# Optimization experiments

Measured on AMD Instinct MI355X. Metric: run time of the kernel, lower is better.

## Reference

```python
import jax, jax.numpy as jnp
import numpy as np
from jax import lax

ASPACE = 500
HEAD = 2
TEMP = 0.8
GEPS = 1e-20
LOG2PI = float(np.log(2.0 * np.pi))


def gru_cell(x, h, Wih, Whh, bih, bhh):
    # torch GRUCell math
    gi = x @ Wih.T + bih
    gh = h @ Whh.T + bhh
    i_r, i_z, i_n = jnp.split(gi, 3, axis=-1)
    h_r, h_z, h_n = jnp.split(gh, 3, axis=-1)
    r = jax.nn.sigmoid(i_r + h_r)
    z = jax.nn.sigmoid(i_z + h_z)
    n = jnp.tanh(i_n + r * h_n)
    return (1.0 - z) * n + z * h


def setup_inputs() -> dict:
    key = jax.random.key(0)
    ks = jax.random.split(key, 16)
    B, T, D, E = 128, 128, 300, 1024
    s = 0.05
    nrm = lambda k, shp: s * jax.random.normal(k, shp, dtype=jnp.float32)
    return {
        "x": jax.random.normal(ks[0], (B, T, D), dtype=jnp.float32),
        "lengths": jnp.full((B,), T, dtype=jnp.int32),  # full-length sequences
        "train": 1,
        # rl_rnn = GRUCell(300, 300)
        "Wih_cell": nrm(ks[1], (3 * D, D)),
        "Whh_cell": nrm(ks[2], (3 * D, D)),
        "bih_cell": nrm(ks[3], (3 * D,)),
        "bhh_cell": nrm(ks[4], (3 * D,)),
        # linear_rl_image_mus: 600 -> 1000
        "Wmu": nrm(ks[5], (ASPACE * HEAD, 2 * D)),
        "bmu": nrm(ks[6], (ASPACE * HEAD,)),
        # linear_logvars: 600 -> 2
        "Wlv": nrm(ks[7], (HEAD, 2 * D)),
        "blv": nrm(ks[8], (HEAD,)),
        # rnn = GRU(300, 1024, 1 layer)
        "Wih_rnn": nrm(ks[9], (3 * E, D)),
        "Whh_rnn": nrm(ks[10], (3 * E, E)),
        "bih_rnn": nrm(ks[11], (3 * E,)),
        "bhh_rnn": nrm(ks[12], (3 * E,)),
        # BatchNorm1d(1024)
        "bn_gamma": jnp.ones((E,), dtype=jnp.float32),
        "bn_beta": jnp.zeros((E,), dtype=jnp.float32),
    }


def _gumbel(key, shape):
    u = jax.random.uniform(key, shape, dtype=jnp.float32)
    return -jnp.log(-jnp.log(u + GEPS) + GEPS)


def reference(x, lengths, train, Wih_cell, Whh_cell, bih_cell, bhh_cell,
              Wmu, bmu, Wlv, blv, Wih_rnn, Whh_rnn, bih_rnn, bhh_rnn,
              bn_gamma, bn_beta):
    # train path only (train==1): stochastic gumbel-softmax + Normal sampling
    B, T, D = x.shape
    E = bn_gamma.shape[0]
    x = lax.stop_gradient(x)  # torch: x = x.detach()

    nk = jax.random.split(jax.random.key(42), 4)
    g_soft = _gumbel(nk[0], (T, B * HEAD, ASPACE))   # gumbel for softmax perturbation
    g_cat = _gumbel(nk[1], (T, B * HEAD, ASPACE))    # gumbel-max trick == multinomial
    eps1 = jax.random.normal(nk[2], (T, B, HEAD), dtype=jnp.float32)  # dist.sample()
    eps2 = jax.random.normal(nk[3], (T, B, HEAD), dtype=jnp.float32)  # second dist.sample() for log_prob

    arange_a = jnp.arange(ASPACE, dtype=jnp.float32)

    def step(hx, inputs):
        img, g, gc, e1, e2 = inputs  # img: [B,300]
        hx = gru_cell(img, hx, Wih_cell, Whh_cell, bih_cell, bhh_cell)
        cat = jax.nn.relu(jnp.concatenate([img, hx], axis=1))  # [B,600]
        mu = cat @ Wmu.T + bmu                                  # [B,1000]
        lv = jax.nn.softplus(cat @ Wlv.T + blv)                 # [B,2]
        logits = mu.reshape(B * HEAD, ASPACE)
        y = jax.nn.softmax((logits + g) / TEMP, axis=-1)
        ind = jnp.argmax(jnp.log(y) + gc, axis=-1)              # multinomial(y, 1)
        prob = jnp.take_along_axis(y, ind[:, None], axis=1)[:, 0]
        one_hot = jax.nn.one_hot(ind, ASPACE, dtype=y.dtype)
        y_hard = lax.stop_gradient(one_hot - y) + y             # straight-through
        action = (arange_a * y_hard).sum(-1).reshape(B, HEAD) / ASPACE  # [B,2]
        std = jnp.exp(0.5 * lv)                                 # [B,2]
        s1 = action + std * e1                                  # img_att sample
        s2 = action + std * e2                                  # sample used in log_prob
        logp = -0.5 * ((s2 - action) / std) ** 2 - jnp.log(std) - 0.5 * LOG2PI
        att = 20.0 * jax.nn.sigmoid(s1)                         # [B,2]
        text = (img.reshape(B, HEAD, D // HEAD) * att[:, :, None]).reshape(B, D)
        return hx, (action, jnp.log(prob).reshape(B, HEAD), logp, text)

    hx0 = jnp.zeros((B, D), dtype=x.dtype)
    xs = (x.transpose(1, 0, 2), g_soft, g_cat, eps1, eps2)
    _, (act, slog, logp, texts) = lax.scan(step, hx0, xs)
    # torch stacking/reshapes
    sampled_log_img_all = slog.transpose(1, 0, 2).reshape(B, HEAD, T)  # stack dim1 then view(B,H,T)
    action_imgs_all = act.transpose(1, 2, 0)                           # [B,2,T]
    log_all = logp.transpose(1, 2, 0)                                  # [B,2,T]

    # second-stage GRU over reconstructed sequence [T,B,300]
    def gru_step(h, xt):
        h = gru_cell(xt, h, Wih_rnn, Whh_rnn, bih_rnn, bhh_rnn)
        return h, h

    _, outs = lax.scan(gru_step, jnp.zeros((B, E), dtype=x.dtype), texts)  # [T,B,E]
    outs = outs.transpose(1, 0, 2)                                         # [B,T,E]
    last = outs[jnp.arange(B), lengths - 1]                                # gather last valid step

    # BatchNorm1d (training mode: batch stats, biased variance)
    mean = last.mean(axis=0)
    var = ((last - mean) ** 2).mean(axis=0)
    feature_end = bn_gamma * (last - mean) / jnp.sqrt(var + 1e-5) + bn_beta
    return (feature_end, sampled_log_img_all, action_imgs_all, log_all)
```

## Files before the change

kernel.cpp:

```cpp
#include <hip/hip_runtime.h>
#include <stdint.h>

#define TT 128
#define BB 128
#define DD 300
#define EE 1024
#define GG 900
#define NMU 1008
#define ASP 500
#define KP 608

#define OUT_SLOG 131072
#define OUT_ACT  163840
#define OUT_LOGP 196608

typedef unsigned int u32x4 __attribute__((ext_vector_type(4)));

__host__ __device__ static inline uint32_t rotl32(uint32_t x, int r){
  return (x << r) | (x >> (32 - r));
}

__host__ __device__ static inline void tf2x32(uint32_t k0, uint32_t k1,
                                              uint32_t x0, uint32_t x1,
                                              uint32_t* o0, uint32_t* o1){
  uint32_t ks2 = k0 ^ k1 ^ 0x1BD11BDAu;
#define TFR(r) { x0 += x1; x1 = rotl32(x1, r); x1 ^= x0; }
  x0 += k0; x1 += k1;
  TFR(13) TFR(15) TFR(26) TFR(6)
  x0 += k1; x1 += ks2 + 1u;
  TFR(17) TFR(29) TFR(16) TFR(24)
  x0 += ks2; x1 += k0 + 2u;
  TFR(13) TFR(15) TFR(26) TFR(6)
  x0 += k0; x1 += k1 + 3u;
  TFR(17) TFR(29) TFR(16) TFR(24)
  x0 += k1; x1 += ks2 + 4u;
  TFR(13) TFR(15) TFR(26) TFR(6)
  x0 += ks2; x1 += k0 + 5u;
#undef TFR
  *o0 = x0; *o1 = x1;
}

__device__ static inline uint32_t rng32(uint32_t k0, uint32_t k1, uint32_t idx){
  uint32_t a, b;
  tf2x32(k0, k1, 0u, idx, &a, &b);
  return a ^ b;
}

__device__ static inline float u01(uint32_t bits){
  return __uint_as_float((bits >> 9) | 0x3f800000u) - 1.0f;
}

__device__ static inline float jgumbel(uint32_t k0, uint32_t k1, uint32_t idx){
  float u = u01(rng32(k0, k1, idx));
  float l1 = logf(u + 1e-20f);
  return -logf(-l1 + 1e-20f);
}

__device__ static inline float erfinv32(float x){
  float w = -log1pf(-x * x);
  float p;
  if (w < 5.0f){
    w = w - 2.5f;
    p = 2.81022636e-08f;
    p = 3.43273939e-07f  + p * w;
    p = -3.5233877e-06f  + p * w;
    p = -4.39150654e-06f + p * w;
    p = 0.00021858087f   + p * w;
    p = -0.00125372503f  + p * w;
    p = -0.00417768164f  + p * w;
    p = 0.246640727f     + p * w;
    p = 1.50140941f      + p * w;
  } else {
    w = sqrtf(w) - 3.0f;
    p = -0.000200214257f;
    p = 0.000100950558f  + p * w;
    p = 0.00134934322f   + p * w;
    p = -0.00367342844f  + p * w;
    p = 0.00573950773f   + p * w;
    p = -0.0076224613f   + p * w;
    p = 0.00943887047f   + p * w;
    p = 1.00167406f      + p * w;
    p = 2.83297682f      + p * w;
  }
  return p * x;
}

__device__ static inline float jnormal(uint32_t k0, uint32_t k1, uint32_t idx){
  float u = u01(rng32(k0, k1, idx));
  const float lo = -0.99999994f;
  float v = u * 2.0f + lo;
  v = fmaxf(lo, v);
  return 1.41421356237f * erfinv32(v);
}

__device__ static inline float jsigmoid(float x){
  return 1.0f / (1.0f + expf(-x));
}

__device__ static inline unsigned short f2bf(float f){
  uint32_t u = __float_as_uint(f);
  uint32_t r = (u + 0x7fffu + ((u >> 16) & 1u)) >> 16;
  return (unsigned short)r;
}
__device__ static inline float bf2f(unsigned short h){
  return __uint_as_float((uint32_t)h << 16);
}

__device__ static inline u32x4 load_b128_llc(const void* p){
  u32x4 r;
  asm volatile("global_load_dwordx4 %0, %1, off sc0 sc1"
               : "=v"(r) : "v"(p) : "memory");
  return r;
}
__device__ static inline void store_b128_llc(void* p, u32x4 v){
  asm volatile("global_store_dwordx4 %0, %1, off sc0 sc1"
               :: "v"(p), "v"(v) : "memory");
}
__device__ static inline unsigned poll_u32_llc(const void* p){
  unsigned r;
  asm volatile("global_load_dword %0, %1, off sc0 sc1\n\ts_waitcnt vmcnt(0)"
               : "=v"(r) : "v"(p) : "memory");
  return r;
}
__device__ static inline void store_u32_llc(void* p, unsigned v){
  asm volatile("global_store_dword %0, %1, off sc0 sc1"
               :: "v"(p), "v"(v) : "memory");
}

#define WAITV(N) do{ asm volatile("s_waitcnt vmcnt(" #N ")" ::: "memory"); \
                     __builtin_amdgcn_sched_barrier(0); }while(0)

#define FMA4(ACC, S, B) { ACC.x += (S)*(B).x; ACC.y += (S)*(B).y; \
                          ACC.z += (S)*(B).z; ACC.w += (S)*(B).w; }

__global__ __launch_bounds__(256) void k_gemm_gi(
    const float* __restrict__ X, const float* __restrict__ W,
    const float* __restrict__ bias, float* __restrict__ C)
{
  __shared__ float As[16][132];
  __shared__ float Bs[16][68];
  const int tid = threadIdx.x;
  const int rbase = blockIdx.y * 128;
  const int cbase = blockIdx.x * 64;
  const int tx = tid & 15, ty = tid >> 4;
  const int sr = tid >> 2, sq = tid & 3;
  const int wj = cbase + sr;

  float4 acc[8];
#pragma unroll
  for (int i = 0; i < 8; ++i) acc[i] = (float4){0,0,0,0};

  for (int k0 = 0; k0 < 304; k0 += 16){
    const int k = k0 + sq * 4;
#pragma unroll
    for (int i = 0; i < 2; ++i){
      const int row = sr + i * 64;
      const int rg = rbase + row;
      float4 va = {0,0,0,0};
      if (k < DD) va = *(const float4*)(X + ((long)(rg & 127) * TT + (rg >> 7)) * DD + k);
      As[sq*4+0][row] = va.x; As[sq*4+1][row] = va.y;
      As[sq*4+2][row] = va.z; As[sq*4+3][row] = va.w;
    }
    {
      float4 vb = {0,0,0,0};
      if (k < DD && wj < GG) vb = *(const float4*)(W + (long)wj * DD + k);
      Bs[sq*4+0][sr] = vb.x; Bs[sq*4+1][sr] = vb.y;
      Bs[sq*4+2][sr] = vb.z; Bs[sq*4+3][sr] = vb.w;
    }
    __syncthreads();
#pragma unroll
    for (int kk = 0; kk < 16; ++kk){
      const float4 b  = *(const float4*)&Bs[kk][tx * 4];
      const float4 a0 = *(const float4*)&As[kk][ty * 8];
      const float4 a1 = *(const float4*)&As[kk][ty * 8 + 4];
      FMA4(acc[0], a0.x, b); FMA4(acc[1], a0.y, b);
      FMA4(acc[2], a0.z, b); FMA4(acc[3], a0.w, b);
      FMA4(acc[4], a1.x, b); FMA4(acc[5], a1.y, b);
      FMA4(acc[6], a1.z, b); FMA4(acc[7], a1.w, b);
    }
    __syncthreads();
  }
  const int ci = cbase + tx * 4;
  float bv[4];
#pragma unroll
  for (int j = 0; j < 4; ++j) bv[j] = (ci + j < GG) ? bias[ci + j] : 0.0f;
#pragma unroll
  for (int i = 0; i < 8; ++i){
    const int r = rbase + ty * 8 + i;
    float vals[4] = {acc[i].x + bv[0], acc[i].y + bv[1],
                     acc[i].z + bv[2], acc[i].w + bv[3]};
    float* crow = C + (long)r * GG;
    if (ci + 3 < GG){
      float4 st = {vals[0], vals[1], vals[2], vals[3]};
      *(float4*)(crow + ci) = st;
    } else {
#pragma unroll
      for (int j = 0; j < 4; ++j) if (ci + j < GG) crow[ci + j] = vals[j];
    }
  }
}

__global__ __launch_bounds__(256) void k_cvt_Amu(
    const float* __restrict__ X, const float* __restrict__ HX,
    unsigned short* __restrict__ Ah, unsigned short* __restrict__ Al)
{
  const long i = (long)blockIdx.x * 256 + threadIdx.x;
  const int r = (int)(i / 152), g = (int)(i - (long)r * 152);
  const int k = g * 4;
  const int b = r & 127, t = r >> 7;
  float4 v = {0,0,0,0};
  if (k < 300)      v = *(const float4*)(X + ((long)b * TT + t) * DD + k);
  else if (k < 600) v = *(const float4*)(HX + (long)r * DD + (k - 300));
  float vv[4] = {fmaxf(v.x,0.f), fmaxf(v.y,0.f), fmaxf(v.z,0.f), fmaxf(v.w,0.f)};
  unsigned short hi[4], lo[4];
#pragma unroll
  for (int j = 0; j < 4; ++j){
    hi[j] = f2bf(vv[j]);
    lo[j] = f2bf(vv[j] - bf2f(hi[j]));
  }
  const long off = (long)r * KP + k;
  *(uint2*)(Ah + off) = *(const uint2*)hi;
  *(uint2*)(Al + off) = *(const uint2*)lo;
}

__global__ __launch_bounds__(256) void k_cvt_Wmu(
    const float* __restrict__ Wmu, const float* __restrict__ Wlv,
    unsigned short* __restrict__ Wh, unsigned short* __restrict__ Wl)
{
  const long i = (long)blockIdx.x * 256 + threadIdx.x;
  const int r = (int)(i / 152), g = (int)(i - (long)r * 152);
  const int k = g * 4;
  float4 v = {0,0,0,0};
  if (k < 600){
    if (r < 1000)      v = *(const float4*)(Wmu + (long)r * 600 + k);
    else if (r < 1002) v = *(const float4*)(Wlv + (long)(r - 1000) * 600 + k);
  }
  float vv[4] = {v.x, v.y, v.z, v.w};
  unsigned short hi[4], lo[4];
#pragma unroll
  for (int j = 0; j < 4; ++j){
    hi[j] = f2bf(vv[j]);
    lo[j] = f2bf(vv[j] - bf2f(hi[j]));
  }
  const long off = (long)r * KP + k;
  *(uint2*)(Wh + off) = *(const uint2*)hi;
  *(uint2*)(Wl + off) = *(const uint2*)lo;
}

__global__ __launch_bounds__(256) void k_bias_mu(
    const float* __restrict__ bmu, const float* __restrict__ blv,
    float* __restrict__ bias)
{
  const int i = blockIdx.x * 256 + threadIdx.x;
  if (i < 1024){
    float v = 0.0f;
    if (i < 1000) v = bmu[i];
    else if (i < 1002) v = blv[i - 1000];
    bias[i] = v;
  }
}

__global__ __launch_bounds__(256) void k_gemm_mf(
    const unsigned short* __restrict__ Ah, const unsigned short* __restrict__ Al,
    const unsigned short* __restrict__ Bh, const unsigned short* __restrict__ Bl,
    const float* __restrict__ bias, float* __restrict__ C)
{
  __shared__ __align__(16) unsigned short sAh[128][40], sAl[128][40];
  __shared__ __align__(16) unsigned short sBh[64][40], sBl[64][40];
  const int tid = threadIdx.x;
  const int cbase = blockIdx.x * 64, rbase = blockIdx.y * 128;
  const int wave = tid >> 6, wm = wave >> 1, wn = wave & 1;
  const int lane = tid & 63, lo = lane & 15, hi4 = lane >> 4;

  using frag = __attribute__((ext_vector_type(8))) short;
  using f32x4 = __attribute__((ext_vector_type(4))) float;
  f32x4 acc[4][2];
#pragma unroll
  for (int a = 0; a < 4; ++a)
#pragma unroll
    for (int c = 0; c < 2; ++c) acc[a][c] = (f32x4){0.f,0.f,0.f,0.f};

  const int arow = tid >> 1, akh = (tid & 1) * 16;
  const int brow = tid >> 2, bkh = (tid & 3) * 8;

  for (int kb = 0; kb < 19; ++kb){
    const int k0 = kb * 32;
    __syncthreads();
    {
      const unsigned short* pa = Ah + (long)(rbase + arow) * KP + k0 + akh;
      *(uint4*)&sAh[arow][akh]     = *(const uint4*)pa;
      *(uint4*)&sAh[arow][akh + 8] = *(const uint4*)(pa + 8);
      const unsigned short* pl = Al + (long)(rbase + arow) * KP + k0 + akh;
      *(uint4*)&sAl[arow][akh]     = *(const uint4*)pl;
      *(uint4*)&sAl[arow][akh + 8] = *(const uint4*)(pl + 8);
      *(uint4*)&sBh[brow][bkh] = *(const uint4*)(Bh + (long)(cbase + brow) * KP + k0 + bkh);
      *(uint4*)&sBl[brow][bkh] = *(const uint4*)(Bl + (long)(cbase + brow) * KP + k0 + bkh);
    }
    __syncthreads();
    frag bh0 = *(const frag*)&sBh[wn*32 + lo][hi4*8];
    frag bh1 = *(const frag*)&sBh[wn*32 + 16 + lo][hi4*8];
    frag bl0 = *(const frag*)&sBl[wn*32 + lo][hi4*8];
    frag bl1 = *(const frag*)&sBl[wn*32 + 16 + lo][hi4*8];
#pragma unroll
    for (int fr = 0; fr < 4; ++fr){
      frag ah = *(const frag*)&sAh[wm*64 + fr*16 + lo][hi4*8];
      frag al = *(const frag*)&sAl[wm*64 + fr*16 + lo][hi4*8];
      acc[fr][0] = __builtin_amdgcn_mfma_f32_16x16x32_bf16(ah, bh0, acc[fr][0], 0, 0, 0);
      acc[fr][0] = __builtin_amdgcn_mfma_f32_16x16x32_bf16(al, bh0, acc[fr][0], 0, 0, 0);
      acc[fr][0] = __builtin_amdgcn_mfma_f32_16x16x32_bf16(ah, bl0, acc[fr][0], 0, 0, 0);
      acc[fr][0] = __builtin_amdgcn_mfma_f32_16x16x32_bf16(al, bl0, acc[fr][0], 0, 0, 0);
      acc[fr][1] = __builtin_amdgcn_mfma_f32_16x16x32_bf16(ah, bh1, acc[fr][1], 0, 0, 0);
      acc[fr][1] = __builtin_amdgcn_mfma_f32_16x16x32_bf16(al, bh1, acc[fr][1], 0, 0, 0);
      acc[fr][1] = __builtin_amdgcn_mfma_f32_16x16x32_bf16(ah, bl1, acc[fr][1], 0, 0, 0);
      acc[fr][1] = __builtin_amdgcn_mfma_f32_16x16x32_bf16(al, bl1, acc[fr][1], 0, 0, 0);
    }
  }
#pragma unroll
  for (int fr = 0; fr < 4; ++fr)
#pragma unroll
    for (int fc = 0; fc < 2; ++fc){
      const int col = cbase + wn*32 + fc*16 + lo;
      if (col < NMU){
        const float bv = bias[col];
        const int r0 = rbase + wm*64 + fr*16 + hi4*4;
#pragma unroll
        for (int j = 0; j < 4; ++j)
          C[(long)(r0 + j) * NMU + col] = acc[fr][fc][j] + bv;
      }
    }
}

__global__ __launch_bounds__(256) void k_pack_whh(
    const float* __restrict__ W, float* __restrict__ Wp)
{
  const int i = blockIdx.x * 256 + threadIdx.x;
  const int kq = i >> 10, j = i & 1023;
  float4 v = {0,0,0,0};
  if (kq < 75 && j < GG){
    const float* s = W + (long)j * DD + kq * 4;
    v.x = s[0]; v.y = s[1]; v.z = s[2]; v.w = s[3];
  }
  *(float4*)(Wp + (long)i * 4) = v;
}

#define S1PAD 304

__global__ __launch_bounds__(256) void k_stage1(
    const float* __restrict__ Wp, const float* __restrict__ bhh,
    const float* __restrict__ gi_all, float* __restrict__ hx_all,
    float* __restrict__ hex, unsigned int* __restrict__ flagsA)
{
  __shared__ __align__(16) float LW[75 * 114 * 4];
  __shared__ __align__(16) float hs[4][S1PAD];
  __shared__ float ghs[4][116];
  const int tid = threadIdx.x;
  const int bid = blockIdx.x;
  const int bq = bid >> 3, js = bid & 7;
  const int b0 = bq * 4;
  const int wid = (js < 4) ? 38 : 37;
  const int jj0 = (js < 4) ? js * 38 : 152 + (js - 4) * 37;
  const int NC = 3 * wid;

  for (int s = tid; s < 75 * NC; s += 256){
    const int kq = s / NC, lc = s - kq * NC;
    const int gate = lc / wid, col = lc - gate * wid;
    const int jcol = gate * 300 + jj0 + col;
    *(float4*)&LW[(kq * 114 + lc) * 4] =
        *(const float4*)(Wp + ((long)kq * 1024 + jcol) * 4);
  }

  const int gc = tid >> 1, rp = tid & 1;
  const bool mact = (gc < NC);

  const bool gact = tid < 4 * wid;
  const int grow = gact ? (tid / wid) : 0;
  const int gcol = gact ? (tid - grow * wid) : 0;
  const int gjj = jj0 + gcol;
  float bhr = 0.f, bhz = 0.f, bhn = 0.f;
  if (gact){ bhr = bhh[gjj]; bhz = bhh[DD + gjj]; bhn = bhh[2*DD + gjj]; }

  for (int i = tid; i < 4 * S1PAD; i += 256) ((float*)hs)[i] = 0.f;
  __syncthreads();

  unsigned int* myflag = flagsA + bid * 16;

  for (int t = 0; t < TT; ++t){
    float gir = 0.f, giz = 0.f, gin = 0.f;
    if (gact){
      const float* gp = gi_all + ((long)t * BB + b0 + grow) * GG;
      gir = gp[gjj]; giz = gp[DD + gjj]; gin = gp[2*DD + gjj];
    }

    if (mact){
      const int r0 = rp * 2, r1 = rp * 2 + 1;
      float4 a0 = {0,0,0,0}, a1 = {0,0,0,0};
#pragma unroll 5
      for (int kq = 0; kq < 75; ++kq){
        const float4 w  = *(const float4*)&LW[(kq * 114 + gc) * 4];
        const float4 h0 = *(const float4*)&hs[r0][kq * 4];
        const float4 h1 = *(const float4*)&hs[r1][kq * 4];
        a0.x = fmaf(w.x, h0.x, a0.x); a0.y = fmaf(w.y, h0.y, a0.y);
        a0.z = fmaf(w.z, h0.z, a0.z); a0.w = fmaf(w.w, h0.w, a0.w);
        a1.x = fmaf(w.x, h1.x, a1.x); a1.y = fmaf(w.y, h1.y, a1.y);
        a1.z = fmaf(w.z, h1.z, a1.z); a1.w = fmaf(w.w, h1.w, a1.w);
      }
      ghs[r0][gc] = (a0.x + a0.y) + (a0.z + a0.w);
      ghs[r1][gc] = (a1.x + a1.y) + (a1.z + a1.w);
    }
    __syncthreads();

    const int par = t & 1;
    if (gact){
      const float r = jsigmoid(gir + ghs[grow][gcol] + bhr);
      const float z = jsigmoid(giz + ghs[grow][wid + gcol] + bhz);
      const float n = tanhf(gin + r * (ghs[grow][2*wid + gcol] + bhn));
      const float hn = (1.0f - z) * n + z * hs[grow][gjj];
      hx_all[((long)t * BB + b0 + grow) * DD + gjj] = hn;
      if (t < TT - 1)
        store_u32_llc(hex + ((long)par * BB + b0 + grow) * S1PAD + gjj,
                      __float_as_uint(hn));
    }

    if (t < TT - 1){
      asm volatile("s_waitcnt vmcnt(0)" ::: "memory");
      __syncthreads();
      if (tid == 0) store_u32_llc(myflag, (unsigned)(t + 1));
      if (tid < 8){
        const unsigned int* fp = flagsA + (bq * 8 + tid) * 16;
        unsigned v = poll_u32_llc(fp);
        while (v < (unsigned)(t + 1)){
          __builtin_amdgcn_s_sleep(1);
          v = poll_u32_llc(fp);
        }
      }
      __syncthreads();
      {
        const float* src = hex + (long)par * BB * S1PAD + (long)b0 * S1PAD;
        const int t0 = tid, t1 = tid + 256;
        const int r0 = t0 / 76, c0 = t0 - r0 * 76;
        u32x4 v0 = load_b128_llc(src + (long)r0 * S1PAD + c0 * 4);
        u32x4 v1 = (u32x4){0,0,0,0};
        int r1 = 0, c1 = 0;
        if (t1 < 304){
          r1 = t1 / 76; c1 = t1 - r1 * 76;
          v1 = load_b128_llc(src + (long)r1 * S1PAD + c1 * 4);
        }
        WAITV(0);
        *(u32x4*)&hs[r0][c0 * 4] = v0;
        if (t1 < 304) *(u32x4*)&hs[r1][c1 * 4] = v1;
      }
      __syncthreads();
    }
  }
}

__global__ __launch_bounds__(256) void k_sample(
    const float* __restrict__ X, const float* __restrict__ mu_all,
    unsigned short* __restrict__ tF, float* __restrict__ out,
    const uint32_t k0a, const uint32_t k0b, const uint32_t k1a, const uint32_t k1b,
    const uint32_t k2a, const uint32_t k2b, const uint32_t k3a, const uint32_t k3b)
{
  const int r = blockIdx.x;
  const int t = r >> 7, b = r & 127;
  const int tid = threadIdx.x;
  const int h = tid >> 7, lane = tid & 127;
  const int wv = tid >> 6;
  __shared__ float redw[4];
  __shared__ int   redi4[4];
  __shared__ float yw[2], lyw[2], att_s[2];

  const uint32_t rowbase = (uint32_t)((t * 256 + b * 2 + h) * 500);
  float zv[4], ev[4];
  float lmax = -3.0e38f;
#pragma unroll
  for (int s = 0; s < 4; ++s){
    const int a = lane + s * 128;
    float z = -3.0e38f;
    if (a < ASP){
      float g = jgumbel(k0a, k0b, rowbase + (uint32_t)a);
      float m = mu_all[(long)r * NMU + h * ASP + a];
      z = (m + g) / 0.8f;
    }
    zv[s] = z;
    lmax = fmaxf(lmax, z);
  }
  {
    float wm = lmax;
#pragma unroll
    for (int o = 32; o > 0; o >>= 1) wm = fmaxf(wm, __shfl_xor(wm, o));
    if ((tid & 63) == 0) redw[wv] = wm;
  }
  __syncthreads();
  const float mx = fmaxf(redw[h * 2], redw[h * 2 + 1]);
  __syncthreads();

  float lsum = 0.0f;
#pragma unroll
  for (int s = 0; s < 4; ++s){
    const int a = lane + s * 128;
    float e = 0.0f;
    if (a < ASP) e = expf(zv[s] - mx);
    ev[s] = e;
    lsum += e;
  }
  {
    float wsum = lsum;
#pragma unroll
    for (int o = 32; o > 0; o >>= 1) wsum += __shfl_xor(wsum, o);
    if ((tid & 63) == 0) redw[wv] = wsum;
  }
  __syncthreads();
  const float S = redw[h * 2] + redw[h * 2 + 1];
  __syncthreads();

  float bestv = -3.0e38f;
  int besti = 0x7fffffff;
#pragma unroll
  for (int s = 0; s < 4; ++s){
    const int a = lane + s * 128;
    if (a < ASP){
      float y = ev[s] / S;
      float ly = logf(y);
      float gc = jgumbel(k1a, k1b, rowbase + (uint32_t)a);
      float val = ly + gc;
      if (val > bestv){ bestv = val; besti = a; }
    }
  }
  {
    float bv = bestv; int bi = besti;
#pragma unroll
    for (int o = 32; o > 0; o >>= 1){
      float v2 = __shfl_xor(bv, o);
      int   i2 = __shfl_xor(bi, o);
      if (v2 > bv || (v2 == bv && i2 < bi)){ bv = v2; bi = i2; }
    }
    if ((tid & 63) == 0){ redw[wv] = bv; redi4[wv] = bi; }
  }
  __syncthreads();
  int ind;
  {
    const float v0 = redw[h * 2], v1 = redw[h * 2 + 1];
    const int   i0 = redi4[h * 2], i1 = redi4[h * 2 + 1];
    ind = (v1 > v0 || (v1 == v0 && i1 < i0)) ? i1 : i0;
  }
#pragma unroll
  for (int s = 0; s < 4; ++s){
    const int a = lane + s * 128;
    if (a == ind){
      float y = ev[s] / S;
      yw[h] = y;
      lyw[h] = logf(y);
    }
  }
  __syncthreads();
  if (lane == 0){
    const float yv = yw[h];
    const float ly = lyw[h];
    const float yh = (1.0f - yv) + yv;
    const float act = ((float)ind * yh) / 500.0f;
    const float lvr = mu_all[(long)r * NMU + 1000 + h];
    const float lv = fmaxf(lvr, 0.0f) + log1pf(expf(-fabsf(lvr)));
    const float sd = expf(0.5f * lv);
    const uint32_t ei = (uint32_t)(r * 2 + h);
    const float e1 = jnormal(k2a, k2b, ei);
    const float e2 = jnormal(k3a, k3b, ei);
    const float s1 = act + sd * e1;
    const float s2 = act + sd * e2;
    const float dd = (s2 - act) / sd;
    const float lp = -0.5f * (dd * dd) - logf(sd) - 0.9189385332046727f;
    const float attv = 20.0f * jsigmoid(s1);
    out[OUT_SLOG + (long)b * 256 + t * 2 + h]  = ly;
    out[OUT_ACT  + (long)b * 256 + h * 128 + t] = act;
    out[OUT_LOGP + (long)b * 256 + h * 128 + t] = lp;
    att_s[h] = attv;
  }
  __syncthreads();
  const float* xr = X + ((long)b * TT + t) * DD;
  if (tid < 40){
    unsigned short pk[8];
#pragma unroll
    for (int e = 0; e < 8; ++e){
      const int idx = tid * 8 + e;
      float v = 0.0f;
      if (idx < 300) v = xr[idx] * att_s[idx / 150];
      pk[e] = f2bf(v);
    }
    unsigned short* dst = tF + (((long)t * 8 + (b >> 4)) * 40 + tid) * 128
                             + (b & 15) * 8;
    *(uint4*)dst = *(const uint4*)pk;
  }
}

__global__ __launch_bounds__(256) void k_cvt_whh(
    const float* __restrict__ W, unsigned short* __restrict__ O)
{
  const int i = blockIdx.x * 256 + threadIdx.x;
  O[i] = f2bf(W[i]);
}

__global__ __launch_bounds__(256) void k_cvt_wih(
    const float* __restrict__ W, unsigned short* __restrict__ O)
{
  const int i = blockIdx.x * 256 + threadIdx.x;
  const int rw = i / 320, c = i - rw * 320;
  O[i] = (c < DD) ? f2bf(W[(long)rw * DD + c]) : (unsigned short)0;
}

#define NBLK2 128
#define WPITCH 2704

__global__ __launch_bounds__(512) void k_stage2(
    const unsigned short* __restrict__ tF,
    const unsigned short* __restrict__ Whb,
    const unsigned short* __restrict__ Wib,
    const float* __restrict__ bih, const float* __restrict__ bhh,
    const int* __restrict__ lengths,
    unsigned short* __restrict__ hF0, unsigned short* __restrict__ hF1,
    float* __restrict__ last,
    unsigned int* __restrict__ flags)
{
  __shared__ __align__(16) char lds[152320];
  unsigned short* Wl = (unsigned short*)lds;
  char* Al = lds + 129792;
  unsigned short* Tl = (unsigned short*)(lds + 150272);

  const int tid = threadIdx.x;
  const int bid = blockIdx.x;
  const int m = bid >> 6, n = bid & 63;
  const int e0 = n * 16, mrow = m * 64;
  const int wave = tid >> 6, wg = wave >> 2, wvr = wave & 3;
  const int lane = tid & 63, lo = lane & 15, hi = lane >> 4;
  const int tidg = tid & 255;

  for (int s = tid; s < 48 * 168; s += 512){
    const int row = s / 168, q = s - row * 168;
    const int g = row >> 4, nn = row & 15;
    const long wrow = (long)g * EE + e0 + nn;
    uint4 v;
    if (q < 128) v = *(const uint4*)(Whb + wrow * EE + q * 8);
    else         v = *(const uint4*)(Wib + wrow * 320 + (q - 128) * 8);
    *(uint4*)((char*)Wl + (long)row * WPITCH + q * 16) = v;
  }

  const int e = e0 + lo;
  const float bR = bih[e] + bhh[e];
  const float bZ = bih[EE + e] + bhh[EE + e];
  const float biN = bih[2*EE + e];
  const float bhN = bhh[2*EE + e];
  int li[4]; float hp[4];
#pragma unroll
  for (int j = 0; j < 4; ++j){
    const int brow = wvr * 16 + hi * 4 + j;
    int l = lengths[mrow + brow] - 1; if (l < 0) l += TT;
    li[j] = l; hp[j] = 0.0f;
  }
  __syncthreads();

  using frag = __attribute__((ext_vector_type(8))) short;
  using f32x4 = __attribute__((ext_vector_type(4))) float;

  const int rg = m * 4 + wvr;
  int boff[3];
#pragma unroll
  for (int g = 0; g < 3; ++g) boff[g] = (g * 16 + lo) * WPITCH + hi * 16;

  const long tBase = ((long)rg * 40 + (wg ? 24 : 0) + hi) * 128 + lo * 8;
  const long hBase = (long)rg * 16384 + (long)(wg * 64 + hi) * 128 + lo * 8;

  unsigned int* flagp = flags + (m << 6) + n;

  for (int t = 0; t < TT; ++t){
    const unsigned short* hFin = (t & 1) ? hF1 : hF0;
    unsigned short* hFout = (t & 1) ? hF0 : hF1;
    const unsigned short* tA = tF + (long)t * 8 * 40 * 128 + tBase;
    const unsigned short* hA = hFin + hBase;

    f32x4 aR = {0,0,0,0}, aZ = {0,0,0,0}, aNH = {0,0,0,0}, aNI = {0,0,0,0};

    auto chunkD = [&](int cc, u32x4 a0v, u32x4 a1v, bool hid){
      frag a0 = *(frag*)&a0v;
      frag a1 = *(frag*)&a1v;
      const char* wb = (const char*)Wl + cc * 128;
      frag b00 = *(const frag*)(wb + boff[0]);
      frag b10 = *(const frag*)(wb + boff[1]);
      frag b20 = *(const frag*)(wb + boff[2]);
      frag b01 = *(const frag*)(wb + boff[0] + 64);
      frag b11 = *(const frag*)(wb + boff[1] + 64);
      frag b21 = *(const frag*)(wb + boff[2] + 64);
      aR = __builtin_amdgcn_mfma_f32_16x16x32_bf16(a0, b00, aR, 0, 0, 0);
      aZ = __builtin_amdgcn_mfma_f32_16x16x32_bf16(a0, b10, aZ, 0, 0, 0);
      if (hid) aNH = __builtin_amdgcn_mfma_f32_16x16x32_bf16(a0, b20, aNH, 0, 0, 0);
      else     aNI = __builtin_amdgcn_mfma_f32_16x16x32_bf16(a0, b20, aNI, 0, 0, 0);
      aR = __builtin_amdgcn_mfma_f32_16x16x32_bf16(a1, b01, aR, 0, 0, 0);
      aZ = __builtin_amdgcn_mfma_f32_16x16x32_bf16(a1, b11, aZ, 0, 0, 0);
      if (hid) aNH = __builtin_amdgcn_mfma_f32_16x16x32_bf16(a1, b21, aNH, 0, 0, 0);
      else     aNI = __builtin_amdgcn_mfma_f32_16x16x32_bf16(a1, b21, aNI, 0, 0, 0);
    };

    {
      u32x4 t0a = load_b128_llc(tA);
      u32x4 t0b = load_b128_llc(tA + 512);
      u32x4 t1a = load_b128_llc(tA + 1024);
      u32x4 t1b = load_b128_llc(tA + 1536);
      if (wg == 0){
        u32x4 t2a = load_b128_llc(tA + 2048);
        u32x4 t2b = load_b128_llc(tA + 2560);
        WAITV(4); chunkD(16, t0a, t0b, false);
        WAITV(2); chunkD(17, t1a, t1b, false);
        WAITV(0); chunkD(18, t2a, t2b, false);
      } else {
        WAITV(2); chunkD(19, t0a, t0b, false);
        WAITV(0); chunkD(20, t1a, t1b, false);
      }
    }

    if (t > 0){
      if (tid < 16){
        const unsigned int* fp = flags + (m << 6) + tid * 4;
        for (;;){
          u32x4 f = load_b128_llc(fp);
          WAITV(0);
          if (f[0] >= (unsigned)t && f[1] >= (unsigned)t &&
              f[2] >= (unsigned)t && f[3] >= (unsigned)t) break;
          __builtin_amdgcn_s_sleep(2);
        }
      }
      __syncthreads();

      u32x4 h0a = load_b128_llc(hA +    0), h0b = load_b128_llc(hA +  512);
      u32x4 h1a = load_b128_llc(hA + 1024), h1b = load_b128_llc(hA + 1536);
      u32x4 h2a = load_b128_llc(hA + 2048), h2b_ = load_b128_llc(hA + 2560);
      u32x4 h3a = load_b128_llc(hA + 3072), h3b = load_b128_llc(hA + 3584);
      u32x4 h4a = load_b128_llc(hA + 4096), h4b = load_b128_llc(hA + 4608);
      u32x4 h5a = load_b128_llc(hA + 5120), h5b = load_b128_llc(hA + 5632);
      u32x4 h6a = load_b128_llc(hA + 6144), h6b = load_b128_llc(hA + 6656);
      u32x4 h7a = load_b128_llc(hA + 7168), h7b = load_b128_llc(hA + 7680);
      const int cb = wg * 8;
      WAITV(14); chunkD(cb + 0, h0a, h0b, true);
      WAITV(12); chunkD(cb + 1, h1a, h1b, true);
      WAITV(10); chunkD(cb + 2, h2a, h2b_, true);
      WAITV(8);  chunkD(cb + 3, h3a, h3b, true);
      WAITV(6);  chunkD(cb + 4, h4a, h4b, true);
      WAITV(4);  chunkD(cb + 5, h5a, h5b, true);
      WAITV(2);  chunkD(cb + 6, h6a, h6b, true);
      WAITV(0);  chunkD(cb + 7, h7a, h7b, true);
    }

    __syncthreads();
    if (wg == 1){
      char* dst = Al + tidg * 80;
      *(f32x4*)(dst)      = aR;
      *(f32x4*)(dst + 16) = aZ;
      *(f32x4*)(dst + 32) = aNH;
      *(f32x4*)(dst + 48) = aNI;
    }
    __syncthreads();
    if (wg == 0){
      const char* src = Al + tidg * 80;
      const f32x4 pR  = *(const f32x4*)(src);
      const f32x4 pZ  = *(const f32x4*)(src + 16);
      const f32x4 pNH = *(const f32x4*)(src + 32);
      const f32x4 pNI = *(const f32x4*)(src + 48);
#pragma unroll
      for (int j = 0; j < 4; ++j){
        aR[j] += pR[j]; aZ[j] += pZ[j]; aNH[j] += pNH[j]; aNI[j] += pNI[j];
      }
#pragma unroll
      for (int j = 0; j < 4; ++j){
        const int brow = wvr * 16 + hi * 4 + j;
        const float r = jsigmoid(aR[j] + bR);
        const float z = jsigmoid(aZ[j] + bZ);
        const float nn2 = tanhf(aNI[j] + biN + r * (aNH[j] + bhN));
        const float hn = (1.0f - z) * nn2 + z * hp[j];
        hp[j] = hn;
        Tl[brow * 16 + lo] = f2bf(hn);
        if (t == li[j]) last[(long)(mrow + brow) * EE + e] = hn;
      }
    }

    if (t < TT - 1){
      __syncthreads();
      if (tid < 128){
        const int rgp = tid >> 5;
        const int kbp = (tid >> 4) & 1;
        const int lop = tid & 15;
        u32x4 v = *(const u32x4*)(Tl + (rgp * 16 + lop) * 16 + kbp * 8);
        store_b128_llc(hFout + ((long)(m * 4 + rgp) * 128 + (n * 2 + kbp)) * 128
                             + lop * 8, v);
      }
      asm volatile("s_waitcnt vmcnt(0)" ::: "memory");
      __syncthreads();
      if (tid == 0) store_u32_llc(flagp, (unsigned)(t + 1));
    }
  }
}

__global__ __launch_bounds__(256) void k_bn_stats(
    const float* __restrict__ last, float* __restrict__ mv)
{
  const int e = blockIdx.x * 256 + threadIdx.x;
  if (e >= EE) return;
  float s = 0.0f;
  for (int b = 0; b < BB; ++b) s += last[(long)b * EE + e];
  const float mean = s / 128.0f;
  float v = 0.0f;
  for (int b = 0; b < BB; ++b){ float d = last[(long)b * EE + e] - mean; v += d * d; }
  mv[e] = mean;
  mv[EE + e] = v / 128.0f;
}

__global__ __launch_bounds__(256) void k_bn_apply(
    const float* __restrict__ last, const float* __restrict__ mv,
    const float* __restrict__ gamma, const float* __restrict__ beta,
    float* __restrict__ out)
{
  const int gid = blockIdx.x * 256 + threadIdx.x;
  const int e = gid & 1023;
  const float xm = last[gid] - mv[e];
  out[gid] = gamma[e] * xm / sqrtf(mv[EE + e] + 1e-5f) + beta[e];
}

extern "C" void kernel_launch(void* const* d_in, const int* in_sizes, int n_in,
                              void* d_out, int out_size, void* d_ws, size_t ws_size,
                              hipStream_t stream)
{
  (void)in_sizes; (void)n_in; (void)out_size;
  const float* x     = (const float*)d_in[0];
  const int*   lens  = (const int*)d_in[1];
  const float* Wih_c = (const float*)d_in[3];
  const float* Whh_c = (const float*)d_in[4];
  const float* bih_c = (const float*)d_in[5];
  const float* bhh_c = (const float*)d_in[6];
  const float* Wmu   = (const float*)d_in[7];
  const float* bmu   = (const float*)d_in[8];
  const float* Wlv   = (const float*)d_in[9];
  const float* blv   = (const float*)d_in[10];
  const float* Wih_r = (const float*)d_in[11];
  const float* Whh_r = (const float*)d_in[12];
  const float* bih_r = (const float*)d_in[13];
  const float* bhh_r = (const float*)d_in[14];
  const float* gam   = (const float*)d_in[15];
  const float* bet   = (const float*)d_in[16];
  float* out = (float*)d_out;

  uint32_t nk[4][2];
  for (uint32_t i = 0; i < 4; ++i) tf2x32(0u, 42u, 0u, i, &nk[i][0], &nk[i][1]);

  float* ws = (float*)d_ws;
  size_t off = 0;
  float* U       = ws + off; off += 16515072;
  float* hx_all  = ws + off; off += 4915200;
  float* Wp      = ws + off; off += 307200;
  float* lastb   = ws + off; off += 131072;
  float* mv      = ws + off; off += 2048;
  float* hex     = ws + off; off += 77824;
  float* biasM   = ws + off; off += 1024;
  unsigned int* flags  = (unsigned int*)(ws + off); off += 2048;
  unsigned int* flagsA = (unsigned int*)(ws + off); off += 4096;
  unsigned short* tF  = (unsigned short*)(ws + off); off += 2621440;
  unsigned short* hF0 = (unsigned short*)(ws + off); off += 65536;
  unsigned short* hF1 = (unsigned short*)(ws + off); off += 65536;
  unsigned short* Whb = (unsigned short*)(ws + off); off += 1572864;
  unsigned short* Wib = (unsigned short*)(ws + off); off += 491520;
  unsigned short* WmH = (unsigned short*)(ws + off); off += 311296;
  unsigned short* WmL = (unsigned short*)(ws + off); off += 311296;
  unsigned short* AmH = (unsigned short*)(ws + off); off += 4980736;
  unsigned short* AmL = (unsigned short*)(ws + off); off += 4980736;
  if (ws_size < off * sizeof(float)) return;

  hipMemsetAsync(flags, 0, 2048 * sizeof(unsigned int), stream);
  hipMemsetAsync(flagsA, 0, 4096 * sizeof(unsigned int), stream);

  k_cvt_whh<<<dim3(12288), 256, 0, stream>>>(Whh_r, Whb);
  k_cvt_wih<<<dim3(3840), 256, 0, stream>>>(Wih_r, Wib);
  k_pack_whh<<<dim3(300), 256, 0, stream>>>(Whh_c, Wp);
  k_cvt_Wmu<<<dim3(608), 256, 0, stream>>>(Wmu, Wlv, WmH, WmL);
  k_bias_mu<<<dim3(4), 256, 0, stream>>>(bmu, blv, biasM);

  k_gemm_gi<<<dim3(15, 128), 256, 0, stream>>>(x, Wih_c, bih_c, U);
  k_stage1<<<dim3(256), 256, 0, stream>>>(Wp, bhh_c, U, hx_all, hex, flagsA);

  k_cvt_Amu<<<dim3(9728), 256, 0, stream>>>(x, hx_all, AmH, AmL);
  k_gemm_mf<<<dim3(16, 128), 256, 0, stream>>>(AmH, AmL, WmH, WmL, biasM, U);
  k_sample<<<dim3(16384), 256, 0, stream>>>(x, U, tF, out,
      nk[0][0], nk[0][1], nk[1][0], nk[1][1],
      nk[2][0], nk[2][1], nk[3][0], nk[3][1]);

  k_stage2<<<dim3(NBLK2), 512, 0, stream>>>(tF, Whb, Wib, bih_r, bhh_r, lens,
                                            hF0, hF1, lastb, flags);

  k_bn_stats<<<dim3(4), 256, 0, stream>>>(lastb, mv);
  k_bn_apply<<<dim3(512), 256, 0, stream>>>(lastb, mv, gam, bet, out);
}
```

Before: 1.635 ms.

## Move stage-1 GRU recurrence matvec to bf16x3 MFMA with register-resident weights

The per-step hidden-state matvec in the first GRU recurrence is rewritten from scalar fp32 FMAs over LDS weights to 16x16x32 bf16 MFMA instructions. Both weights and hidden state are split into three bf16 terms to keep roughly fp32 accuracy. Weights are pre-split by a new pack kernel and held in registers. The block decomposition changes from 4 batch rows by 8 column slices to 8 rows by 16 slices, so each block polls 16 flags per step. Each step now also converts the exchanged hidden state into bf16 triples, and the nine MFMAs per k-slice plus the extra flag polling add per-step latency.

```diff
diff --git a/kernel.cpp b/kernel.cpp
--- a/kernel.cpp
+++ b/kernel.cpp
@@ -330,56 +330,82 @@
     }
 }
 
-__global__ __launch_bounds__(256) void k_pack_whh(
-    const float* __restrict__ W, float* __restrict__ Wp)
-{
-  const int i = blockIdx.x * 256 + threadIdx.x;
-  const int kq = i >> 10, j = i & 1023;
-  float4 v = {0,0,0,0};
-  if (kq < 75 && j < GG){
-    const float* s = W + (long)j * DD + kq * 4;
-    v.x = s[0]; v.y = s[1]; v.z = s[2]; v.w = s[3];
-  }
-  *(float4*)(Wp + (long)i * 4) = v;
+__global__ __launch_bounds__(256) void k_pack_w3(
+    const float* __restrict__ W, unsigned short* __restrict__ Wb3)
+{
+  const int g = blockIdx.x * 256 + threadIdx.x;
+  if (g >= 245760) return;
+  const int k4 = g % 80;
+  const int r2 = g / 80;
+  const int row = r2 % 64;
+  const int r3 = r2 / 64;
+  const int s = r3 % 3;
+  const int js = r3 / 3;
+  const int wid = (js < 15) ? 19 : 15;
+  const int jj0 = js * 19;
+  unsigned short o4[4];
+#pragma unroll
+  for (int e = 0; e < 4; ++e){
+    const int k = k4 * 4 + e;
+    float v = 0.0f;
+    if (row < 3 * wid && k < 300){
+      const int gate = row / wid, col = row - gate * wid;
+      v = W[(long)(gate * 300 + jj0 + col) * 300 + k];
+    }
+    const unsigned short w1 = f2bf(v);
+    const float r1 = v - bf2f(w1);
+    const unsigned short w2 = f2bf(r1);
+    const float r2f = r1 - bf2f(w2);
+    const unsigned short w3 = f2bf(r2f);
+    o4[e] = (s == 0) ? w1 : ((s == 1) ? w2 : w3);
+  }
+  *(uint2*)(Wb3 + ((long)(js * 3 + s) * 64 + row) * 320 + k4 * 4) = *(const uint2*)o4;
 }
 
 #define S1PAD 304
 
-__global__ __launch_bounds__(256) void k_stage1(
-    const float* __restrict__ Wp, const float* __restrict__ bhh,
+__global__ __launch_bounds__(256, 1) void k_stage1(
+    const unsigned short* __restrict__ Wb3, const float* __restrict__ bhh,
     const float* __restrict__ gi_all, float* __restrict__ hx_all,
     float* __restrict__ hex, unsigned int* __restrict__ flagsA)
 {
-  __shared__ __align__(16) float LW[75 * 114 * 4];
-  __shared__ __align__(16) float hs[4][S1PAD];
-  __shared__ float ghs[4][116];
+  __shared__ __align__(16) float hs[8][S1PAD];
+  __shared__ __align__(16) unsigned short hb[3][8][320];
+  __shared__ float ghs[512];
   const int tid = threadIdx.x;
   const int bid = blockIdx.x;
-  const int bq = bid >> 3, js = bid & 7;
-  const int b0 = bq * 4;
-  const int wid = (js < 4) ? 38 : 37;
-  const int jj0 = (js < 4) ? js * 38 : 152 + (js - 4) * 37;
+  const int bq = bid >> 4, js = bid & 15;
+  const int b0 = bq * 8;
+  const int wid = (js < 15) ? 19 : 15;
+  const int jj0 = js * 19;
   const int NC = 3 * wid;
 
-  for (int s = tid; s < 75 * NC; s += 256){
-    const int kq = s / NC, lc = s - kq * NC;
-    const int gate = lc / wid, col = lc - gate * wid;
-    const int jcol = gate * 300 + jj0 + col;
-    *(float4*)&LW[(kq * 114 + lc) * 4] =
-        *(const float4*)(Wp + ((long)kq * 1024 + jcol) * 4);
-  }
-
-  const int gc = tid >> 1, rp = tid & 1;
-  const bool mact = (gc < NC);
-
-  const bool gact = tid < 4 * wid;
+  const int wave = tid >> 6, lane = tid & 63;
+  const int lo = lane & 15, hi = lane >> 4;
+
+  using frag = __attribute__((ext_vector_type(8))) short;
+  using f32x4v = __attribute__((ext_vector_type(4))) float;
+
+  frag wfr[3][10];
+  {
+    const int row = wave * 16 + lo;
+#pragma unroll
+    for (int s = 0; s < 3; ++s)
+#pragma unroll
+      for (int kf = 0; kf < 10; ++kf)
+        wfr[s][kf] = *(const frag*)(Wb3 + ((long)(js * 3 + s) * 64 + row) * 320
+                                         + kf * 32 + hi * 8);
+  }
+
+  const bool gact = tid < 8 * wid;
   const int grow = gact ? (tid / wid) : 0;
   const int gcol = gact ? (tid - grow * wid) : 0;
   const int gjj = jj0 + gcol;
   float bhr = 0.f, bhz = 0.f, bhn = 0.f;
   if (gact){ bhr = bhh[gjj]; bhz = bhh[DD + gjj]; bhn = bhh[2*DD + gjj]; }
 
-  for (int i = tid; i < 4 * S1PAD; i += 256) ((float*)hs)[i] = 0.f;
+  for (int i = tid; i < 8 * S1PAD; i += 256) ((float*)hs)[i] = 0.f;
+  for (int i = tid; i < 3840; i += 256) ((unsigned int*)hb)[i] = 0u;
   __syncthreads();
 
   unsigned int* myflag = flagsA + bid * 16;
@@ -391,29 +417,37 @@
       gir = gp[gjj]; giz = gp[DD + gjj]; gin = gp[2*DD + gjj];
     }
 
-    if (mact){
-      const int r0 = rp * 2, r1 = rp * 2 + 1;
-      float4 a0 = {0,0,0,0}, a1 = {0,0,0,0};
-#pragma unroll 5
-      for (int kq = 0; kq < 75; ++kq){
-        const float4 w  = *(const float4*)&LW[(kq * 114 + gc) * 4];
-        const float4 h0 = *(const float4*)&hs[r0][kq * 4];
-        const float4 h1 = *(const float4*)&hs[r1][kq * 4];
-        a0.x = fmaf(w.x, h0.x, a0.x); a0.y = fmaf(w.y, h0.y, a0.y);
-        a0.z = fmaf(w.z, h0.z, a0.z); a0.w = fmaf(w.w, h0.w, a0.w);
-        a1.x = fmaf(w.x, h1.x, a1.x); a1.y = fmaf(w.y, h1.y, a1.y);
-        a1.z = fmaf(w.z, h1.z, a1.z); a1.w = fmaf(w.w, h1.w, a1.w);
+    f32x4v a0 = {0,0,0,0}, a1 = {0,0,0,0}, a2 = {0,0,0,0};
+#pragma unroll
+    for (int kf = 0; kf < 10; ++kf){
+      frag h1 = *(const frag*)&hb[0][lo & 7][kf * 32 + hi * 8];
+      frag h2 = *(const frag*)&hb[1][lo & 7][kf * 32 + hi * 8];
+      frag h3 = *(const frag*)&hb[2][lo & 7][kf * 32 + hi * 8];
+      a0 = __builtin_amdgcn_mfma_f32_16x16x32_bf16(h1, wfr[0][kf], a0, 0, 0, 0);
+      a1 = __builtin_amdgcn_mfma_f32_16x16x32_bf16(h1, wfr[1][kf], a1, 0, 0, 0);
+      a2 = __builtin_amdgcn_mfma_f32_16x16x32_bf16(h1, wfr[2][kf], a2, 0, 0, 0);
+      a0 = __builtin_amdgcn_mfma_f32_16x16x32_bf16(h2, wfr[0][kf], a0, 0, 0, 0);
+      a1 = __builtin_amdgcn_mfma_f32_16x16x32_bf16(h2, wfr[1][kf], a1, 0, 0, 0);
+      a2 = __builtin_amdgcn_mfma_f32_16x16x32_bf16(h2, wfr[2][kf], a2, 0, 0, 0);
+      a0 = __builtin_amdgcn_mfma_f32_16x16x32_bf16(h3, wfr[0][kf], a0, 0, 0, 0);
+      a1 = __builtin_amdgcn_mfma_f32_16x16x32_bf16(h3, wfr[1][kf], a1, 0, 0, 0);
+      a2 = __builtin_amdgcn_mfma_f32_16x16x32_bf16(h3, wfr[2][kf], a2, 0, 0, 0);
+    }
+    {
+      const int nc = wave * 16 + lo;
+      if (hi < 2 && nc < NC){
+#pragma unroll
+        for (int j = 0; j < 4; ++j)
+          ghs[nc * 8 + hi * 4 + j] = (a0[j] + a1[j]) + a2[j];
       }
-      ghs[r0][gc] = (a0.x + a0.y) + (a0.z + a0.w);
-      ghs[r1][gc] = (a1.x + a1.y) + (a1.z + a1.w);
     }
     __syncthreads();
 
     const int par = t & 1;
     if (gact){
-      const float r = jsigmoid(gir + ghs[grow][gcol] + bhr);
-      const float z = jsigmoid(giz + ghs[grow][wid + gcol] + bhz);
-      const float n = tanhf(gin + r * (ghs[grow][2*wid + gcol] + bhn));
+      const float r = jsigmoid(gir + ghs[(0 * wid + gcol) * 8 + grow] + bhr);
+      const float z = jsigmoid(giz + ghs[(1 * wid + gcol) * 8 + grow] + bhz);
+      const float n = tanhf(gin + r * (ghs[(2 * wid + gcol) * 8 + grow] + bhn));
       const float hn = (1.0f - z) * n + z * hs[grow][gjj];
       hx_all[((long)t * BB + b0 + grow) * DD + gjj] = hn;
       if (t < TT - 1)
@@ -425,8 +459,8 @@
       asm volatile("s_waitcnt vmcnt(0)" ::: "memory");
       __syncthreads();
       if (tid == 0) store_u32_llc(myflag, (unsigned)(t + 1));
-      if (tid < 8){
-        const unsigned int* fp = flagsA + (bq * 8 + tid) * 16;
+      if (tid < 16){
+        const unsigned int* fp = flagsA + (bq * 16 + tid) * 16;
         unsigned v = poll_u32_llc(fp);
         while (v < (unsigned)(t + 1)){
           __builtin_amdgcn_s_sleep(1);
@@ -436,18 +470,40 @@
       __syncthreads();
       {
         const float* src = hex + (long)par * BB * S1PAD + (long)b0 * S1PAD;
-        const int t0 = tid, t1 = tid + 256;
-        const int r0 = t0 / 76, c0 = t0 - r0 * 76;
-        u32x4 v0 = load_b128_llc(src + (long)r0 * S1PAD + c0 * 4);
-        u32x4 v1 = (u32x4){0,0,0,0};
-        int r1 = 0, c1 = 0;
-        if (t1 < 304){
-          r1 = t1 / 76; c1 = t1 - r1 * 76;
-          v1 = load_b128_llc(src + (long)r1 * S1PAD + c1 * 4);
+        const int gA = tid, gB = tid + 256, gC = tid + 512;
+        const int rA = gA / 76, cA = gA - rA * 76;
+        const int rB = gB / 76, cB = gB - rB * 76;
+        int rC = 0, cC = 0;
+        u32x4 vA = load_b128_llc(src + (long)rA * S1PAD + cA * 4);
+        u32x4 vB = load_b128_llc(src + (long)rB * S1PAD + cB * 4);
+        u32x4 vC = (u32x4){0,0,0,0};
+        if (gC < 608){
+          rC = gC / 76; cC = gC - rC * 76;
+          vC = load_b128_llc(src + (long)rC * S1PAD + cC * 4);
         }
         WAITV(0);
-        *(u32x4*)&hs[r0][c0 * 4] = v0;
-        if (t1 < 304) *(u32x4*)&hs[r1][c1 * 4] = v1;
+#define CONV_STORE(rr, cc, vv) do{ \
+        float f0 = __uint_as_float(vv[0]), f1 = __uint_as_float(vv[1]); \
+        float f2v = __uint_as_float(vv[2]), f3 = __uint_as_float(vv[3]); \
+        if ((cc) == 75){ f0 = 0.f; f1 = 0.f; f2v = 0.f; f3 = 0.f; } \
+        *(u32x4*)&hs[rr][(cc) * 4] = vv; \
+        float fv[4] = {f0, f1, f2v, f3}; \
+        unsigned short s1[4], s2[4], s3[4]; \
+        _Pragma("unroll") \
+        for (int j = 0; j < 4; ++j){ \
+          s1[j] = f2bf(fv[j]); \
+          const float r1 = fv[j] - bf2f(s1[j]); \
+          s2[j] = f2bf(r1); \
+          s3[j] = f2bf(r1 - bf2f(s2[j])); \
+        } \
+        *(uint2*)&hb[0][rr][(cc) * 4] = *(const uint2*)s1; \
+        *(uint2*)&hb[1][rr][(cc) * 4] = *(const uint2*)s2; \
+        *(uint2*)&hb[2][rr][(cc) * 4] = *(const uint2*)s3; \
+      }while(0)
+        CONV_STORE(rA, cA, vA);
+        CONV_STORE(rB, cB, vB);
+        if (gC < 608) CONV_STORE(rC, cC, vC);
+#undef CONV_STORE
       }
       __syncthreads();
     }
@@ -850,7 +906,6 @@
   size_t off = 0;
   float* U       = ws + off; off += 16515072;
   float* hx_all  = ws + off; off += 4915200;
-  float* Wp      = ws + off; off += 307200;
   float* lastb   = ws + off; off += 131072;
   float* mv      = ws + off; off += 2048;
   float* hex     = ws + off; off += 77824;
@@ -862,6 +917,7 @@
   unsigned short* hF1 = (unsigned short*)(ws + off); off += 65536;
   unsigned short* Whb = (unsigned short*)(ws + off); off += 1572864;
   unsigned short* Wib = (unsigned short*)(ws + off); off += 491520;
+  unsigned short* Wb3 = (unsigned short*)(ws + off); off += 491520;
   unsigned short* WmH = (unsigned short*)(ws + off); off += 311296;
   unsigned short* WmL = (unsigned short*)(ws + off); off += 311296;
   unsigned short* AmH = (unsigned short*)(ws + off); off += 4980736;
@@ -873,12 +929,12 @@
 
   k_cvt_whh<<<dim3(12288), 256, 0, stream>>>(Whh_r, Whb);
   k_cvt_wih<<<dim3(3840), 256, 0, stream>>>(Wih_r, Wib);
-  k_pack_whh<<<dim3(300), 256, 0, stream>>>(Whh_c, Wp);
+  k_pack_w3<<<dim3(960), 256, 0, stream>>>(Whh_c, Wb3);
   k_cvt_Wmu<<<dim3(608), 256, 0, stream>>>(Wmu, Wlv, WmH, WmL);
   k_bias_mu<<<dim3(4), 256, 0, stream>>>(bmu, blv, biasM);
 
   k_gemm_gi<<<dim3(15, 128), 256, 0, stream>>>(x, Wih_c, bih_c, U);
-  k_stage1<<<dim3(256), 256, 0, stream>>>(Wp, bhh_c, U, hx_all, hex, flagsA);
+  k_stage1<<<dim3(256), 256, 0, stream>>>(Wb3, bhh_c, U, hx_all, hex, flagsA);
 
   k_cvt_Amu<<<dim3(9728), 256, 0, stream>>>(x, hx_all, AmH, AmL);
   k_gemm_mf<<<dim3(16, 128), 256, 0, stream>>>(AmH, AmL, WmH, WmL, biasM, U);
```

New measurement: 1.493 ms. -8.7%, faster.
